# Kernel tuning notes

Measured on AMD Instinct MI355X. Metric: run time of the kernel, lower is better.

The kernel has to match this reference:

```python
import jax, jax.numpy as jnp
import numpy as np

DROPOUT_P = 0.5


def normalize_adj(A):
    # A_tilda = A + I ; A_hat = D^-0.5 A_tilda D^-0.5
    # The torch code does this with diag_embed + two bmm (O(N^3));
    # mathematically it is row/col broadcasting (O(N^2)).
    B, N, _ = A.shape
    A_tilda = A + jnp.eye(N, dtype=A.dtype)
    d_inv_sqrt = jnp.sum(A_tilda, axis=2) ** -0.5          # [B, N]
    return d_inv_sqrt[:, :, None] * A_tilda * d_inv_sqrt[:, None, :]


def gcn_layer(X, A_hat, W, b):
    # standard Kipf GCN layer: A_hat @ (X @ W) + b
    return jnp.einsum('bnm,bmd->bnd', A_hat, X @ W) + b


def setup_inputs() -> dict:
    key = jax.random.key(0)
    ks = jax.random.split(key, 6)
    B, N, Din, H, C = 8, 2048, 64, 64, 16
    X = jax.random.normal(ks[0], (B, N, Din), dtype=jnp.float32)
    A = jax.random.uniform(ks[1], (B, N, N), dtype=jnp.float32)
    W1 = jax.random.normal(ks[2], (Din, H), dtype=jnp.float32) * (1.0 / np.sqrt(Din))
    b1 = jax.random.normal(ks[3], (H,), dtype=jnp.float32) * 0.01
    W2 = jax.random.normal(ks[4], (H, C), dtype=jnp.float32) * (1.0 / np.sqrt(H))
    b2 = jax.random.normal(ks[5], (C,), dtype=jnp.float32) * 0.01
    return {"X": X, "A": A, "W1": W1, "b1": b1, "W2": W2, "b2": b2}


def reference(X, A, W1, b1, W2, b2):
    A_hat = normalize_adj(A)
    h = jax.nn.relu(gcn_layer(X, A_hat, W1, b1))
    # F.dropout default training=True -> apply dropout with a fixed key
    keep = jax.random.bernoulli(jax.random.key(42), 1.0 - DROPOUT_P, h.shape)
    h = jnp.where(keep, h / (1.0 - DROPOUT_P), 0.0).astype(h.dtype)
    return gcn_layer(h, A_hat, W2, b2)
```

## Files before the change

kernel.cpp:

```cpp
#include <hip/hip_runtime.h>

#define BN 16384
#define NN 2048
#define DD 64
#define CC 16
#define KS1 8
#define KS2 16

typedef short bf16x8 __attribute__((ext_vector_type(8)));
typedef float f32x4 __attribute__((ext_vector_type(4)));
typedef unsigned short u16x4 __attribute__((ext_vector_type(4)));

__device__ __forceinline__ f32x4 mfma16(bf16x8 a, bf16x8 b, f32x4 c) {
  return __builtin_amdgcn_mfma_f32_16x16x32_bf16(a, b, c, 0, 0, 0);
}
__device__ __forceinline__ unsigned short f2bf(float f) {
  unsigned u = __float_as_uint(f);
  return (unsigned short)((u + 0x7FFFu + ((u >> 16) & 1u)) >> 16);
}
__device__ __forceinline__ float bf2f(unsigned short h) {
  return __uint_as_float(((unsigned)h) << 16);
}

__device__ __forceinline__ unsigned tf_bits(unsigned i) {
  unsigned x0 = 0u;
  unsigned x1 = i;
  const unsigned k0 = 0u, k1 = 42u, k2 = 0x1BD11BDAu ^ 0u ^ 42u;
  x0 += k0; x1 += k1;
#define TFR(r) { x0 += x1; x1 = (x1 << (r)) | (x1 >> (32 - (r))); x1 ^= x0; }
  TFR(13) TFR(15) TFR(26) TFR(6)
  x0 += k1; x1 += k2 + 1u;
  TFR(17) TFR(29) TFR(16) TFR(24)
  x0 += k2; x1 += k0 + 2u;
  TFR(13) TFR(15) TFR(26) TFR(6)
  x0 += k0; x1 += k1 + 3u;
  TFR(17) TFR(29) TFR(16) TFR(24)
  x0 += k1; x1 += k2 + 4u;
  TFR(13) TFR(15) TFR(26) TFR(6)
  x0 += k2; x1 += k0 + 5u;
#undef TFR
  return x0 ^ x1;
}


__global__ __launch_bounds__(256) void k_deg(const float* __restrict__ A,
    const float* __restrict__ X, const float* __restrict__ W1,
    float* __restrict__ dis, unsigned short* __restrict__ Abf,
    unsigned short* __restrict__ Y1s, unsigned short* __restrict__ Y1sT)
{
  const int w = threadIdx.x >> 6, lane = threadIdx.x & 63;
  const size_t row = (size_t)blockIdx.x * 4 + w;
  const float4* Arow = (const float4*)(A + row * NN);
  unsigned short* Brow = Abf + row * NN;
  float s = 0.f;
#pragma unroll
  for (int it = 0; it < 8; ++it) {
    float4 v = Arow[lane + 64 * it];
    s += (v.x + v.y) + (v.z + v.w);
    u16x4 p = { f2bf(v.x), f2bf(v.y), f2bf(v.z), f2bf(v.w) };
    *(u16x4*)(Brow + lane * 4 + it * 256) = p;
  }
#pragma unroll
  for (int m = 32; m; m >>= 1) s += __shfl_xor(s, m, 64);
  const float dv = 1.0f / sqrtf(s + 1.0f);
  if (lane == 0) dis[row] = dv;
  const float* Xr = X + row * DD;
  float acc = 0.f;
#pragma unroll
  for (int k = 0; k < DD; ++k) acc += Xr[k] * W1[k * DD + lane];
  const unsigned short yv = f2bf(dv * acc);
  Y1s[row * DD + lane] = yv;
  const int b = (int)(row >> 11), kr = (int)(row & (NN - 1));
  Y1sT[((size_t)b * DD + lane) * NN + kr] = yv;
}

__global__ __launch_bounds__(256, 4) void k_gemm1(const unsigned short* __restrict__ Abf,
    const unsigned short* __restrict__ Y1sT, float* __restrict__ Z1)
{
  const int Mb = blockIdx.x >> 4;
  const int ns = (blockIdx.x >> 3) & 1;
  const int ks = blockIdx.x & 7;
  const int w = __builtin_amdgcn_readfirstlane((int)threadIdx.x >> 6);
  const int lane = threadIdx.x & 63;
  const int m15 = lane & 15, quad = lane >> 4;
  const int b = Mb >> 3;
  const int k0 = ks * 256 + quad * 8;
  const unsigned short* Ap[4];
#pragma unroll
  for (int m = 0; m < 4; ++m)
    Ap[m] = Abf + ((size_t)Mb * 256 + m * 64 + w * 16 + m15) * NN + k0;
  const unsigned short* Bp0 = Y1sT + ((size_t)b * DD + ns * 32 + m15) * NN + k0;
  const unsigned short* Bp1 = Bp0 + (size_t)16 * NN;
  const f32x4 zero = 0.f;
  f32x4 acc[4][2];
#pragma unroll
  for (int m = 0; m < 4; ++m) { acc[m][0] = zero; acc[m][1] = zero; }
  bf16x8 a[4], b0, b1;
#pragma unroll
  for (int m = 0; m < 4; ++m) a[m] = *(const bf16x8*)Ap[m];
  b0 = *(const bf16x8*)Bp0;
  b1 = *(const bf16x8*)Bp1;
#pragma unroll 1
  for (int kk = 0; kk < 8; ++kk) {
    const int off = (kk < 7) ? (kk + 1) * 32 : 0;
    bf16x8 na[4], nb0, nb1;
#pragma unroll
    for (int m = 0; m < 4; ++m) na[m] = *(const bf16x8*)(Ap[m] + off);
    nb0 = *(const bf16x8*)(Bp0 + off);
    nb1 = *(const bf16x8*)(Bp1 + off);
#pragma unroll
    for (int m = 0; m < 4; ++m) {
      acc[m][0] = mfma16(a[m], b0, acc[m][0]);
      acc[m][1] = mfma16(a[m], b1, acc[m][1]);
    }
#pragma unroll
    for (int m = 0; m < 4; ++m) a[m] = na[m];
    b0 = nb0; b1 = nb1;
  }
#pragma unroll
  for (int m = 0; m < 4; ++m)
#pragma unroll
    for (int t = 0; t < 2; ++t)
#pragma unroll
      for (int r = 0; r < 4; ++r)
        Z1[((size_t)ks * BN + Mb * 256 + m * 64 + w * 16 + quad * 4 + r) * DD
           + ns * 32 + t * 16 + m15] = acc[m][t][r];
}

__global__ __launch_bounds__(256) void k_epi1(const float* __restrict__ Z1,
    const unsigned short* __restrict__ Y1s, const float* __restrict__ dis,
    const float* __restrict__ b1, const float* __restrict__ W2,
    unsigned short* __restrict__ Y2sT)
{
  __shared__ float hs[16][65];
  __shared__ float W2l[DD * CC];
  const int tid = threadIdx.x;
  *(float4*)(W2l + tid * 4) = *(const float4*)(W2 + tid * 4);
  const int r0 = blockIdx.x * 16;
#pragma unroll
  for (int j = 0; j < 4; ++j) {
    const int e = tid + j * 256;
    const int rl = e >> 6, n = e & 63;
    const size_t row = (size_t)r0 + rl;
    const size_t o = row * DD + n;
    float z = bf2f(Y1s[o]);
#pragma unroll
    for (int p = 0; p < KS1; ++p) z += Z1[((size_t)p * BN + row) * DD + n];
    float h = fmaxf(dis[row] * z + b1[n], 0.f);
    const unsigned bits = tf_bits((unsigned)o);
    hs[rl][n] = (bits >> 31) ? 0.f : (h + h);
  }
  __syncthreads();
  const int c = tid & 15, rl = tid >> 4;
  float s = 0.f;
#pragma unroll
  for (int k = 0; k < DD; ++k) s += hs[rl][k] * W2l[k * CC + c];
  const int row = r0 + rl;
  const int b = row >> 11, kr = row & (NN - 1);
  Y2sT[((size_t)b * CC + c) * NN + kr] = f2bf(dis[row] * s);
}

__global__ __launch_bounds__(256, 4) void k_gemm2(const unsigned short* __restrict__ Abf,
    const unsigned short* __restrict__ Y2sT, float* __restrict__ Z2)
{
  const int Mb = blockIdx.x >> 4;
  const int ks = blockIdx.x & 15;
  const int w = __builtin_amdgcn_readfirstlane((int)threadIdx.x >> 6);
  const int lane = threadIdx.x & 63;
  const int m15 = lane & 15, quad = lane >> 4;
  const int b = Mb >> 3;
  const int k0 = ks * 128 + quad * 8;
  const unsigned short* Ap[4];
#pragma unroll
  for (int m = 0; m < 4; ++m)
    Ap[m] = Abf + ((size_t)Mb * 256 + m * 64 + w * 16 + m15) * NN + k0;
  const unsigned short* Bp = Y2sT + ((size_t)b * CC + m15) * NN + k0;
  const f32x4 zero = 0.f;
  f32x4 acc[4];
#pragma unroll
  for (int m = 0; m < 4; ++m) acc[m] = zero;
  bf16x8 a[4], bb;
#pragma unroll
  for (int m = 0; m < 4; ++m) a[m] = *(const bf16x8*)Ap[m];
  bb = *(const bf16x8*)Bp;
#pragma unroll 1
  for (int kk = 0; kk < 4; ++kk) {
    const int off = (kk < 3) ? (kk + 1) * 32 : 0;
    bf16x8 na[4], nbb;
#pragma unroll
    for (int m = 0; m < 4; ++m) na[m] = *(const bf16x8*)(Ap[m] + off);
    nbb = *(const bf16x8*)(Bp + off);
#pragma unroll
    for (int m = 0; m < 4; ++m) acc[m] = mfma16(a[m], bb, acc[m]);
#pragma unroll
    for (int m = 0; m < 4; ++m) a[m] = na[m];
    bb = nbb;
  }
#pragma unroll
  for (int m = 0; m < 4; ++m)
#pragma unroll
    for (int r = 0; r < 4; ++r)
      Z2[((size_t)ks * BN + Mb * 256 + m * 64 + w * 16 + quad * 4 + r) * CC + m15] = acc[m][r];
}

__global__ __launch_bounds__(256) void k_final(const float* __restrict__ Z2,
    const unsigned short* __restrict__ Y2sT, const float* __restrict__ dis,
    const float* __restrict__ b2, float* __restrict__ out)
{
  const int gid = blockIdx.x * 256 + threadIdx.x;
  const int r = gid >> 2, q = gid & 3;
  const int b = r >> 11, kr = r & (NN - 1);
  float4 s;
  s.x = bf2f(Y2sT[((size_t)b * CC + q * 4 + 0) * NN + kr]);
  s.y = bf2f(Y2sT[((size_t)b * CC + q * 4 + 1) * NN + kr]);
  s.z = bf2f(Y2sT[((size_t)b * CC + q * 4 + 2) * NN + kr]);
  s.w = bf2f(Y2sT[((size_t)b * CC + q * 4 + 3) * NN + kr]);
#pragma unroll
  for (int p = 0; p < KS2; ++p) {
    const float4 zp = *(const float4*)(Z2 + ((size_t)p * BN + r) * CC + q * 4);
    s.x += zp.x; s.y += zp.y; s.z += zp.z; s.w += zp.w;
  }
  const float dv = dis[r];
  const float4 bb = *(const float4*)(b2 + q * 4);
  float4 res;
  res.x = dv * s.x + bb.x;
  res.y = dv * s.y + bb.y;
  res.z = dv * s.z + bb.z;
  res.w = dv * s.w + bb.w;
  *(float4*)(out + (size_t)r * CC + q * 4) = res;
}

#define FKS1 4
#define FKS2 16

__global__ __launch_bounds__(256) void d_deg_xw(const float* __restrict__ A,
    const float* __restrict__ X, const float* __restrict__ W1,
    float* __restrict__ dis, float* __restrict__ Y1s)
{
  const int w = threadIdx.x >> 6, lane = threadIdx.x & 63;
  const int row = __builtin_amdgcn_readfirstlane(blockIdx.x * 4 + w);
  const float4* Arow = (const float4*)(A + (size_t)row * NN);
  float s = 0.f;
#pragma unroll
  for (int it = 0; it < 8; ++it) {
    float4 v = Arow[lane + 64 * it];
    s += v.x + v.y + v.z + v.w;
  }
#pragma unroll
  for (int m = 32; m; m >>= 1) s += __shfl_xor(s, m, 64);
  const float dv = 1.0f / sqrtf(s + 1.0f);
  if (lane == 0) dis[row] = dv;
  const float* Xr = X + (size_t)row * DD;
  float acc = 0.f;
#pragma unroll
  for (int k = 0; k < DD; ++k) acc += Xr[k] * W1[k * DD + lane];
  Y1s[(size_t)row * DD + lane] = dv * acc;
}

__global__ __launch_bounds__(256) void d_gemm1(const float* __restrict__ A,
    const float* __restrict__ Y1s, float* __restrict__ Z1)
{
  const int rb = blockIdx.x >> 2, ks = blockIdx.x & (FKS1 - 1);
  const int lane = threadIdx.x & 63;
  const int c0 = __builtin_amdgcn_readfirstlane((threadIdx.x >> 6) << 4);
  const int row = rb * 64 + lane;
  const int batch = rb >> 5;
  const int KSEG = NN / FKS1;
  const float* Arow = A + (size_t)row * NN + ks * KSEG;
  const float* Yb = Y1s + (size_t)batch * NN * DD + c0;
  const int kbase = ks * KSEG;
  float acc[16];
#pragma unroll
  for (int c = 0; c < 16; ++c) acc[c] = 0.f;
  float4 a0 = *(const float4*)(Arow);
  float4 a1 = *(const float4*)(Arow + 4);
  float4 a2 = *(const float4*)(Arow + 8);
  float4 a3 = *(const float4*)(Arow + 12);
  for (int k = 0; k < KSEG; k += 16) {
    const int kn = (k + 16 < KSEG) ? (k + 16) : 0;
    float4 n0 = *(const float4*)(Arow + kn);
    float4 n1 = *(const float4*)(Arow + kn + 4);
    float4 n2 = *(const float4*)(Arow + kn + 8);
    float4 n3 = *(const float4*)(Arow + kn + 12);
    const float* y0 = Yb + (size_t)(kbase + k) * DD;
    const float av[16] = {a0.x, a0.y, a0.z, a0.w, a1.x, a1.y, a1.z, a1.w,
                          a2.x, a2.y, a2.z, a2.w, a3.x, a3.y, a3.z, a3.w};
#pragma unroll
    for (int j = 0; j < 16; ++j) {
      const float* yr = y0 + j * DD;
#pragma unroll
      for (int c = 0; c < 16; ++c) acc[c] += av[j] * yr[c];
    }
    a0 = n0; a1 = n1; a2 = n2; a3 = n3;
  }
  float* Zp = Z1 + ((size_t)ks * BN + row) * DD + c0;
#pragma unroll
  for (int c = 0; c < 16; c += 4) {
    float4 v; v.x = acc[c]; v.y = acc[c+1]; v.z = acc[c+2]; v.w = acc[c+3];
    *(float4*)(Zp + c) = v;
  }
}

__global__ __launch_bounds__(256) void d_epi1(const float* __restrict__ Z1,
    const float* __restrict__ Y1s, const float* __restrict__ dis,
    const float* __restrict__ b1, const float* __restrict__ W2,
    float* __restrict__ Y2s)
{
  __shared__ float W2l[DD * CC];
  __shared__ float hl[4][DD];
  const int tid = threadIdx.x;
  *(float4*)(W2l + tid * 4) = *(const float4*)(W2 + tid * 4);
  const int w = tid >> 6, lane = tid & 63;
  const int row = blockIdx.x * 4 + w;
  const size_t o = (size_t)row * DD + lane;
  float z = Y1s[o];
#pragma unroll
  for (int p = 0; p < FKS1; ++p) z += Z1[(size_t)p * BN * DD + o];
  const float dv = dis[row];
  float h = fmaxf(dv * z + b1[lane], 0.f);
  const unsigned bits = tf_bits((unsigned)o);
  h = (bits >> 31) ? 0.f : (h + h);
  hl[w][lane] = h;
  __syncthreads();
  const int wr = tid >> 6, l = tid & 63;
  const int c = l & 15, kq = l >> 4;
  float p = 0.f;
#pragma unroll
  for (int kk = 0; kk < 16; ++kk)
    p += hl[wr][kq * 16 + kk] * W2l[(kq * 16 + kk) * CC + c];
  p += __shfl_xor(p, 16, 64);
  p += __shfl_xor(p, 32, 64);
  if (l < 16) {
    const int rg = blockIdx.x * 4 + wr;
    Y2s[(size_t)rg * CC + c] = dis[rg] * p;
  }
}

__global__ __launch_bounds__(256) void d_gemm2(const float* __restrict__ A,
    const float* __restrict__ Y2s, float* __restrict__ Z2)
{
  const int rb = blockIdx.x >> 4, ks = blockIdx.x & (FKS2 - 1);
  const int row = rb * 256 + threadIdx.x;
  const int batch = rb >> 3;
  const int KSEG = NN / FKS2;
  const float* Arow = A + (size_t)row * NN + ks * KSEG;
  const float* Yb = Y2s + (size_t)batch * NN * CC;
  const int kbase = ks * KSEG;
  float acc[16];
#pragma unroll
  for (int c = 0; c < 16; ++c) acc[c] = 0.f;
  float4 a0 = *(const float4*)(Arow);
  float4 a1 = *(const float4*)(Arow + 4);
  for (int k = 0; k < KSEG; k += 8) {
    const int kn = (k + 8 < KSEG) ? (k + 8) : 0;
    float4 n0 = *(const float4*)(Arow + kn);
    float4 n1 = *(const float4*)(Arow + kn + 4);
    const float av[8] = {a0.x, a0.y, a0.z, a0.w, a1.x, a1.y, a1.z, a1.w};
#pragma unroll
    for (int j = 0; j < 8; ++j) {
      const float* yr = Yb + (size_t)(kbase + k + j) * CC;
#pragma unroll
      for (int c = 0; c < 16; ++c) acc[c] += av[j] * yr[c];
    }
    a0 = n0; a1 = n1;
  }
  float* Zp = Z2 + ((size_t)ks * BN + row) * CC;
#pragma unroll
  for (int c = 0; c < 16; c += 4) {
    float4 v; v.x = acc[c]; v.y = acc[c+1]; v.z = acc[c+2]; v.w = acc[c+3];
    *(float4*)(Zp + c) = v;
  }
}

__global__ __launch_bounds__(256) void d_final(const float* __restrict__ Z2,
    const float* __restrict__ Y2s, const float* __restrict__ dis,
    const float* __restrict__ b2, float* __restrict__ out)
{
  const int gid = blockIdx.x * 256 + threadIdx.x;
  const int r = gid >> 2, q = gid & 3;
  const size_t o = (size_t)r * CC + q * 4;
  float4 s = *(const float4*)(Y2s + o);
#pragma unroll
  for (int p = 0; p < FKS2; ++p) {
    const float4 zp = *(const float4*)(Z2 + (size_t)p * BN * CC + o);
    s.x += zp.x; s.y += zp.y; s.z += zp.z; s.w += zp.w;
  }
  const float dv = dis[r];
  const float4 bb = *(const float4*)(b2 + q * 4);
  float4 res;
  res.x = dv * s.x + bb.x;
  res.y = dv * s.y + bb.y;
  res.z = dv * s.z + bb.z;
  res.w = dv * s.w + bb.w;
  *(float4*)(out + o) = res;
}

extern "C" void kernel_launch(void* const* d_in, const int* in_sizes, int n_in,
                              void* d_out, int out_size, void* d_ws, size_t ws_size,
                              hipStream_t stream) {
  const float* X  = (const float*)d_in[0];
  const float* A  = (const float*)d_in[1];
  const float* W1 = (const float*)d_in[2];
  const float* b1 = (const float*)d_in[3];
  const float* W2 = (const float*)d_in[4];
  const float* b2 = (const float*)d_in[5];
  float* out = (float*)d_out;
  char* wsb = (char*)d_ws;

  const size_t NEED = 105447424;
  if (ws_size >= NEED) {
    unsigned short* Abf  = (unsigned short*)wsb;
    float*          Z1   = (float*)(wsb + 67108864);
    float*          Z2   = Z1;
    float*          dis  = (float*)(wsb + 100663296);
    unsigned short* Y1s  = (unsigned short*)(wsb + 100728832);
    unsigned short* Y1sT = (unsigned short*)(wsb + 102825984);
    unsigned short* Y2sT = (unsigned short*)(wsb + 104923136);

    k_deg  <<<BN / 4,  256, 0, stream>>>(A, X, W1, dis, Abf, Y1s, Y1sT);
    k_gemm1<<<1024,    256, 0, stream>>>(Abf, Y1sT, Z1);
    k_epi1 <<<BN / 16, 256, 0, stream>>>(Z1, Y1s, dis, b1, W2, Y2sT);
    k_gemm2<<<1024,    256, 0, stream>>>(Abf, Y2sT, Z2);
    k_final<<<256,     256, 0, stream>>>(Z2, Y2sT, dis, b2, out);
  } else {
    float* ws  = (float*)d_ws;
    float* dis = ws;
    float* Y1s = ws + 16384;
    float* Z1  = Y1s + (size_t)BN * DD;
    float* Z2  = Z1;
    float* Y2s = Z1 + (size_t)FKS1 * BN * DD;

    d_deg_xw<<<BN / 4,     256, 0, stream>>>(A, X, W1, dis, Y1s);
    d_gemm1 <<<256 * FKS1, 256, 0, stream>>>(A, Y1s, Z1);
    d_epi1  <<<BN / 4,     256, 0, stream>>>(Z1, Y1s, dis, b1, W2, Y2s);
    d_gemm2 <<<64 * FKS2,  256, 0, stream>>>(A, Y2s, Z2);
    d_final <<<256,        256, 0, stream>>>(Z2, Y2s, dis, b2, out);
  }
}
```

Before: 274.6 us.

## Replace split-K partial buffers with float atomicAdd accumulation

The split-K GEMM kernels previously wrote per-split partial results to large Z buffers, and the epilogue and final kernels then summed them. Now both GEMMs atomically add into a single accumulator: S1 is zeroed up front, and S2 is seeded with the self-loop term by the epilogue. This removes the partial-buffer writes and re-reads, at the cost of an extra zero kernel, atomic contention and non-deterministic summation order.

```diff
diff --git a/kernel.cpp b/kernel.cpp
--- a/kernel.cpp
+++ b/kernel.cpp
@@ -43,6 +43,12 @@
 }
 
 
+__global__ __launch_bounds__(256) void k_zero(float* __restrict__ S)
+{
+  const f32x4 z = 0.f;
+  ((f32x4*)S)[blockIdx.x * 256 + threadIdx.x] = z;
+}
+
 __global__ __launch_bounds__(256) void k_deg(const float* __restrict__ A,
     const float* __restrict__ X, const float* __restrict__ W1,
     float* __restrict__ dis, unsigned short* __restrict__ Abf,
@@ -75,7 +81,7 @@
 }
 
 __global__ __launch_bounds__(256, 4) void k_gemm1(const unsigned short* __restrict__ Abf,
-    const unsigned short* __restrict__ Y1sT, float* __restrict__ Z1)
+    const unsigned short* __restrict__ Y1sT, float* __restrict__ S1)
 {
   const int Mb = blockIdx.x >> 4;
   const int ns = (blockIdx.x >> 3) & 1;
@@ -123,14 +129,14 @@
     for (int t = 0; t < 2; ++t)
 #pragma unroll
       for (int r = 0; r < 4; ++r)
-        Z1[((size_t)ks * BN + Mb * 256 + m * 64 + w * 16 + quad * 4 + r) * DD
-           + ns * 32 + t * 16 + m15] = acc[m][t][r];
-}
-
-__global__ __launch_bounds__(256) void k_epi1(const float* __restrict__ Z1,
+        atomicAdd(&S1[((size_t)Mb * 256 + m * 64 + w * 16 + quad * 4 + r) * DD
+                      + ns * 32 + t * 16 + m15], acc[m][t][r]);
+}
+
+__global__ __launch_bounds__(256) void k_epi1(const float* __restrict__ S1,
     const unsigned short* __restrict__ Y1s, const float* __restrict__ dis,
     const float* __restrict__ b1, const float* __restrict__ W2,
-    unsigned short* __restrict__ Y2sT)
+    unsigned short* __restrict__ Y2sT, float* __restrict__ S2)
 {
   __shared__ float hs[16][65];
   __shared__ float W2l[DD * CC];
@@ -143,9 +149,7 @@
     const int rl = e >> 6, n = e & 63;
     const size_t row = (size_t)r0 + rl;
     const size_t o = row * DD + n;
-    float z = bf2f(Y1s[o]);
-#pragma unroll
-    for (int p = 0; p < KS1; ++p) z += Z1[((size_t)p * BN + row) * DD + n];
+    const float z = bf2f(Y1s[o]) + S1[o];
     float h = fmaxf(dis[row] * z + b1[n], 0.f);
     const unsigned bits = tf_bits((unsigned)o);
     hs[rl][n] = (bits >> 31) ? 0.f : (h + h);
@@ -157,11 +161,13 @@
   for (int k = 0; k < DD; ++k) s += hs[rl][k] * W2l[k * CC + c];
   const int row = r0 + rl;
   const int b = row >> 11, kr = row & (NN - 1);
-  Y2sT[((size_t)b * CC + c) * NN + kr] = f2bf(dis[row] * s);
+  const float y2 = dis[row] * s;
+  Y2sT[((size_t)b * CC + c) * NN + kr] = f2bf(y2);
+  S2[(size_t)row * CC + c] = y2;
 }
 
 __global__ __launch_bounds__(256, 4) void k_gemm2(const unsigned short* __restrict__ Abf,
-    const unsigned short* __restrict__ Y2sT, float* __restrict__ Z2)
+    const unsigned short* __restrict__ Y2sT, float* __restrict__ S2)
 {
   const int Mb = blockIdx.x >> 4;
   const int ks = blockIdx.x & 15;
@@ -200,26 +206,18 @@
   for (int m = 0; m < 4; ++m)
 #pragma unroll
     for (int r = 0; r < 4; ++r)
-      Z2[((size_t)ks * BN + Mb * 256 + m * 64 + w * 16 + quad * 4 + r) * CC + m15] = acc[m][r];
-}
-
-__global__ __launch_bounds__(256) void k_final(const float* __restrict__ Z2,
-    const unsigned short* __restrict__ Y2sT, const float* __restrict__ dis,
-    const float* __restrict__ b2, float* __restrict__ out)
+      atomicAdd(&S2[((size_t)Mb * 256 + m * 64 + w * 16 + quad * 4 + r) * CC + m15],
+                acc[m][r]);
+}
+
+__global__ __launch_bounds__(256) void k_final(const float* __restrict__ S2,
+    const float* __restrict__ dis, const float* __restrict__ b2,
+    float* __restrict__ out)
 {
   const int gid = blockIdx.x * 256 + threadIdx.x;
   const int r = gid >> 2, q = gid & 3;
-  const int b = r >> 11, kr = r & (NN - 1);
-  float4 s;
-  s.x = bf2f(Y2sT[((size_t)b * CC + q * 4 + 0) * NN + kr]);
-  s.y = bf2f(Y2sT[((size_t)b * CC + q * 4 + 1) * NN + kr]);
-  s.z = bf2f(Y2sT[((size_t)b * CC + q * 4 + 2) * NN + kr]);
-  s.w = bf2f(Y2sT[((size_t)b * CC + q * 4 + 3) * NN + kr]);
-#pragma unroll
-  for (int p = 0; p < KS2; ++p) {
-    const float4 zp = *(const float4*)(Z2 + ((size_t)p * BN + r) * CC + q * 4);
-    s.x += zp.x; s.y += zp.y; s.z += zp.z; s.w += zp.w;
-  }
+  const size_t o = (size_t)r * CC + q * 4;
+  const float4 s = *(const float4*)(S2 + o);
   const float dv = dis[r];
   const float4 bb = *(const float4*)(b2 + q * 4);
   float4 res;
@@ -227,7 +225,7 @@
   res.y = dv * s.y + bb.y;
   res.z = dv * s.z + bb.z;
   res.w = dv * s.w + bb.w;
-  *(float4*)(out + (size_t)r * CC + q * 4) = res;
+  *(float4*)(out + o) = res;
 }
 
 #define FKS1 4
@@ -407,21 +405,22 @@
   float* out = (float*)d_out;
   char* wsb = (char*)d_ws;
 
-  const size_t NEED = 105447424;
+  const size_t NEED = 77135872;
   if (ws_size >= NEED) {
     unsigned short* Abf  = (unsigned short*)wsb;
-    float*          Z1   = (float*)(wsb + 67108864);
-    float*          Z2   = Z1;
-    float*          dis  = (float*)(wsb + 100663296);
-    unsigned short* Y1s  = (unsigned short*)(wsb + 100728832);
-    unsigned short* Y1sT = (unsigned short*)(wsb + 102825984);
-    unsigned short* Y2sT = (unsigned short*)(wsb + 104923136);
-
+    float*          S1   = (float*)(wsb + 67108864);
+    float*          S2   = (float*)(wsb + 71303168);
+    float*          dis  = (float*)(wsb + 72351744);
+    unsigned short* Y1s  = (unsigned short*)(wsb + 72417280);
+    unsigned short* Y1sT = (unsigned short*)(wsb + 74514432);
+    unsigned short* Y2sT = (unsigned short*)(wsb + 76611584);
+
+    k_zero <<<1280,    256, 0, stream>>>(S1);
     k_deg  <<<BN / 4,  256, 0, stream>>>(A, X, W1, dis, Abf, Y1s, Y1sT);
-    k_gemm1<<<1024,    256, 0, stream>>>(Abf, Y1sT, Z1);
-    k_epi1 <<<BN / 16, 256, 0, stream>>>(Z1, Y1s, dis, b1, W2, Y2sT);
-    k_gemm2<<<1024,    256, 0, stream>>>(Abf, Y2sT, Z2);
-    k_final<<<256,     256, 0, stream>>>(Z2, Y2sT, dis, b2, out);
+    k_gemm1<<<1024,    256, 0, stream>>>(Abf, Y1sT, S1);
+    k_epi1 <<<BN / 16, 256, 0, stream>>>(S1, Y1s, dis, b1, W2, Y2sT, S2);
+    k_gemm2<<<1024,    256, 0, stream>>>(Abf, Y2sT, S2);
+    k_final<<<256,     256, 0, stream>>>(S2, dis, b2, out);
   } else {
     float* ws  = (float*)d_ws;
     float* dis = ws;
```

Result: slower. 295.9 us (+7.7%).
